# Performance work log

Measured on AMD Instinct MI355X. Metric: run time of the kernel, lower is better.

The kernel has to match this reference:

```python
import jax, jax.numpy as jnp
import numpy as np

T, N, E, H, G, P = 8, 512, 64, 128, 4, 128
NS = 2.0  # neighbourhood_size


def _init(k, shape):
    fan_in = shape[-1]
    return jax.random.normal(k, shape, jnp.float32) / jnp.sqrt(jnp.float32(fan_in))


def setup_inputs() -> dict:
    key = jax.random.key(0)
    ks = jax.random.split(key, 12)
    return {
        "observed": jax.random.normal(ks[0], (T, N, 2), jnp.float32),
        "W_pos": _init(ks[1], (E, 2)), "b_pos": jnp.zeros((E,), jnp.float32),
        "W_pool": _init(ks[2], (P, G * G * H)), "b_pool": jnp.zeros((P,), jnp.float32),
        "W_ih_enc": _init(ks[3], (4 * H, E + P)), "b_ih_enc": jnp.zeros((4 * H,), jnp.float32),
        "W_hh_enc": _init(ks[4], (4 * H, H)), "b_hh_enc": jnp.zeros((4 * H,), jnp.float32),
        "W_ih_dec": _init(ks[5], (4 * H, E + P)), "b_ih_dec": jnp.zeros((4 * H,), jnp.float32),
        "W_hh_dec": _init(ks[6], (4 * H, H)), "b_hh_dec": jnp.zeros((4 * H,), jnp.float32),
        "W_out": _init(ks[7], (2, H)), "b_out": jnp.zeros((2,), jnp.float32),
        "n_predict": 12,
    }


def _impute(observed):
    # backfill leading gaps, forward-fill later gaps, zeros if never valid
    Tn, n, _ = observed.shape
    finite = jnp.isfinite(observed).all(-1)                       # [T,N]
    idx = jnp.where(finite, jnp.arange(Tn)[:, None], -1)
    last = jax.lax.associative_scan(jnp.maximum, idx, axis=0)     # last valid t' <= t
    first = jnp.argmax(finite, axis=0)                            # first valid t
    take = jnp.where(last >= 0, last, first[None, :])             # [T,N]
    obs = jnp.take_along_axis(observed, jnp.broadcast_to(take[:, :, None], (Tn, n, 2)), axis=0)
    return jnp.where(finite.any(0)[None, :, None], obs, 0.0)


def _social_pool(pos, hidden, W_pool, b_pool):
    # grid-cell binning + per-cell max pooling of neighbour hidden states
    n, h = hidden.shape
    half, cell = NS / 2.0, NS / G
    rel = pos[None, :, :] - pos[:, None, :]                       # [N,N,2] pos[j]-pos[i]
    fin_pos = jnp.isfinite(pos).all(-1)
    fin_hid = jnp.isfinite(hidden).all(-1)
    inr = (jnp.abs(rel) <= half).all(-1)
    eye = jnp.eye(n, dtype=bool)
    mask = inr & fin_pos[:, None] & fin_pos[None, :] & fin_hid[None, :] & (~eye)
    g = jnp.clip(jnp.floor((rel + half) / cell).astype(jnp.int32), 0, G - 1)  # [N,N,2]
    cid = g[..., 0] * G + g[..., 1]                               # gx*G+gy layout
    seg = jnp.where(mask, jnp.arange(n, dtype=jnp.int32)[:, None] * (G * G) + cid, n * G * G)
    seg = seg.reshape(-1)                                         # [N*N]
    data = jnp.broadcast_to(hidden[None], (n, n, h)).reshape(n * n, h)
    pooled = jax.ops.segment_max(data, seg, num_segments=n * G * G + 1)[: n * G * G]
    counts = jax.ops.segment_sum(jnp.ones((n * n,), jnp.float32), seg, num_segments=n * G * G + 1)[: n * G * G]
    pooled = jnp.where(counts[:, None] > 0, pooled, 0.0)          # empty cells -> zero_hidden
    grid = pooled.reshape(n, G * G * h)
    return jax.nn.relu(grid @ W_pool.T + b_pool)


def reference(observed, W_pos, b_pos, W_pool, b_pool,
              W_ih_enc, b_ih_enc, W_hh_enc, b_hh_enc,
              W_ih_dec, b_ih_dec, W_hh_dec, b_hh_dec,
              W_out, b_out, n_predict):
    obs = _impute(observed)
    n = obs.shape[1]

    def step(W_ih, b_ih, W_hh, b_hh, hs, cs, pos, prev):
        vel = pos - prev
        emb = jax.nn.relu(vel @ W_pos.T + b_pos)
        soc = _social_pool(pos, hs, W_pool, b_pool)
        x = jnp.concatenate([emb, soc], axis=1)
        gates = x @ W_ih.T + b_ih + hs @ W_hh.T + b_hh
        i, f, gg, o = jnp.split(gates, 4, axis=1)
        cs2 = jax.nn.sigmoid(f) * cs + jax.nn.sigmoid(i) * jnp.tanh(gg)
        hs2 = jax.nn.sigmoid(o) * jnp.tanh(cs2)
        nxt = pos + hs2 @ W_out.T + b_out
        return hs2, cs2, nxt

    def enc_step(carry, inp):
        hs, cs = carry
        pos, prev = inp
        hs, cs, _ = step(W_ih_enc, b_ih_enc, W_hh_enc, b_hh_enc, hs, cs, pos, prev)
        return (hs, cs), None

    hs = jnp.zeros((n, H), jnp.float32)
    cs = jnp.zeros((n, H), jnp.float32)
    (hs, cs), _ = jax.lax.scan(enc_step, (hs, cs), (obs[1:], obs[:-1]))

    def dec_step(carry, _):
        hs, cs, prev, curr = carry
        hs, cs, nxt = step(W_ih_dec, b_ih_dec, W_hh_dec, b_hh_dec, hs, cs, curr, prev)
        return (hs, cs, jax.lax.stop_gradient(curr), jax.lax.stop_gradient(nxt)), nxt

    _, preds = jax.lax.scan(dec_step, (hs, cs, obs[-1], obs[-1]), None, length=int(n_predict))
    return preds  # [n_predict, N, 2]
```

## Files before the change

kernel.cpp:

```cpp
#include <hip/hip_runtime.h>
#include <math.h>

#define NBLK 256
#define NTHR 512

#define OFF_OBS     8256
#define OFF_HS      16448
#define OFF_PART    81984
#define OFF_WTPOOL  606272
#define OFF_WTG_E   868416
#define OFF_WTG_D   1032256

#define LDS_BYTES 31232

typedef float vf4 __attribute__((ext_vector_type(4)));
typedef float vf2 __attribute__((ext_vector_type(2)));

__device__ __forceinline__ int asr20(int row) { return row * 20 + ((row >> 5) << 2); }

__device__ __forceinline__ void st_bypass_f4(float* p, vf4 v) {
    asm volatile("global_store_dwordx4 %0, %1, off sc0 sc1" :: "v"(p), "v"(v) : "memory");
}
__device__ __forceinline__ void st_bypass_f2(float* p, vf2 v) {
    asm volatile("global_store_dwordx2 %0, %1, off sc0 sc1" :: "v"(p), "v"(v) : "memory");
}
__device__ __forceinline__ vf4 ld_bypass_f4(const float* p) {
    vf4 v;
    asm volatile("global_load_dwordx4 %0, %1, off sc0 sc1\n\ts_waitcnt vmcnt(0)"
                 : "=&v"(v) : "v"(p) : "memory");
    return v;
}
__device__ __forceinline__ void ld_bypass_f4x8(const float* b, int stride, vf4* v) {
    asm volatile(
        "global_load_dwordx4 %0, %8, off sc0 sc1\n\t"
        "global_load_dwordx4 %1, %9, off sc0 sc1\n\t"
        "global_load_dwordx4 %2, %10, off sc0 sc1\n\t"
        "global_load_dwordx4 %3, %11, off sc0 sc1\n\t"
        "global_load_dwordx4 %4, %12, off sc0 sc1\n\t"
        "global_load_dwordx4 %5, %13, off sc0 sc1\n\t"
        "global_load_dwordx4 %6, %14, off sc0 sc1\n\t"
        "global_load_dwordx4 %7, %15, off sc0 sc1\n\t"
        "s_waitcnt vmcnt(0)"
        : "=&v"(v[0]), "=&v"(v[1]), "=&v"(v[2]), "=&v"(v[3]),
          "=&v"(v[4]), "=&v"(v[5]), "=&v"(v[6]), "=&v"(v[7])
        : "v"(b), "v"(b + stride), "v"(b + 2 * stride), "v"(b + 3 * stride),
          "v"(b + 4 * stride), "v"(b + 5 * stride), "v"(b + 6 * stride), "v"(b + 7 * stride)
        : "memory");
}
__device__ __forceinline__ void ld_gather8(
    const float* a0, const float* a1, const float* a2, const float* a3,
    const float* a4, const float* a5, const float* a6, const float* a7, vf4* v) {
    asm volatile(
        "global_load_dwordx4 %0, %16, off sc0 sc1\n\t"
        "global_load_dwordx4 %1, %16, off offset:16 sc0 sc1\n\t"
        "global_load_dwordx4 %2, %17, off sc0 sc1\n\t"
        "global_load_dwordx4 %3, %17, off offset:16 sc0 sc1\n\t"
        "global_load_dwordx4 %4, %18, off sc0 sc1\n\t"
        "global_load_dwordx4 %5, %18, off offset:16 sc0 sc1\n\t"
        "global_load_dwordx4 %6, %19, off sc0 sc1\n\t"
        "global_load_dwordx4 %7, %19, off offset:16 sc0 sc1\n\t"
        "global_load_dwordx4 %8, %20, off sc0 sc1\n\t"
        "global_load_dwordx4 %9, %20, off offset:16 sc0 sc1\n\t"
        "global_load_dwordx4 %10, %21, off sc0 sc1\n\t"
        "global_load_dwordx4 %11, %21, off offset:16 sc0 sc1\n\t"
        "global_load_dwordx4 %12, %22, off sc0 sc1\n\t"
        "global_load_dwordx4 %13, %22, off offset:16 sc0 sc1\n\t"
        "global_load_dwordx4 %14, %23, off sc0 sc1\n\t"
        "global_load_dwordx4 %15, %23, off offset:16 sc0 sc1\n\t"
        "s_waitcnt vmcnt(0)"
        : "=&v"(v[0]), "=&v"(v[1]), "=&v"(v[2]), "=&v"(v[3]),
          "=&v"(v[4]), "=&v"(v[5]), "=&v"(v[6]), "=&v"(v[7]),
          "=&v"(v[8]), "=&v"(v[9]), "=&v"(v[10]), "=&v"(v[11]),
          "=&v"(v[12]), "=&v"(v[13]), "=&v"(v[14]), "=&v"(v[15])
        : "v"(a0), "v"(a1), "v"(a2), "v"(a3), "v"(a4), "v"(a5), "v"(a6), "v"(a7)
        : "memory");
}
__device__ __forceinline__ float ld_cohere(const float* p) {
    return __hip_atomic_load(p, __ATOMIC_RELAXED, __HIP_MEMORY_SCOPE_AGENT);
}

__device__ __forceinline__ void grid_barrier_fenced(unsigned* flags, unsigned* gen, unsigned seq) {
    __syncthreads();
    if (threadIdx.x == 0)
        __builtin_amdgcn_fence(__ATOMIC_RELEASE, "agent");
    if (blockIdx.x == 0) {
        if (threadIdx.x < 64) {
            #pragma unroll
            for (int q = 0; q < 4; q++) {
                int bb = threadIdx.x * 4 + q;
                if (bb != 0) {
                    while (__hip_atomic_load(&flags[bb * 16], __ATOMIC_RELAXED,
                                             __HIP_MEMORY_SCOPE_AGENT) != seq)
                        __builtin_amdgcn_s_sleep(1);
                }
            }
        }
        __syncthreads();
        if (threadIdx.x == 0) {
            __hip_atomic_store(gen, seq, __ATOMIC_RELAXED, __HIP_MEMORY_SCOPE_AGENT);
            __builtin_amdgcn_fence(__ATOMIC_ACQUIRE, "agent");
        }
    } else {
        if (threadIdx.x == 0) {
            __hip_atomic_store(&flags[blockIdx.x * 16], seq, __ATOMIC_RELAXED,
                               __HIP_MEMORY_SCOPE_AGENT);
            while (__hip_atomic_load(gen, __ATOMIC_RELAXED,
                                     __HIP_MEMORY_SCOPE_AGENT) != seq)
                __builtin_amdgcn_s_sleep(2);
            __builtin_amdgcn_fence(__ATOMIC_ACQUIRE, "agent");
        }
    }
    __syncthreads();
}

__device__ __forceinline__ void grid_barrier_nf(unsigned* flags, unsigned* gen, unsigned seq) {
    __syncthreads();
    if (blockIdx.x == 0) {
        if (threadIdx.x < 64) {
            #pragma unroll
            for (int q = 0; q < 4; q++) {
                int bb = threadIdx.x * 4 + q;
                if (bb != 0) {
                    while (__hip_atomic_load(&flags[bb * 16], __ATOMIC_RELAXED,
                                             __HIP_MEMORY_SCOPE_AGENT) != seq)
                        __builtin_amdgcn_s_sleep(1);
                }
            }
        }
        __syncthreads();
        if (threadIdx.x == 0)
            __hip_atomic_store(gen, seq, __ATOMIC_RELAXED, __HIP_MEMORY_SCOPE_AGENT);
    } else {
        if (threadIdx.x == 0) {
            __hip_atomic_store(&flags[blockIdx.x * 16], seq, __ATOMIC_RELAXED,
                               __HIP_MEMORY_SCOPE_AGENT);
            while (__hip_atomic_load(gen, __ATOMIC_RELAXED,
                                     __HIP_MEMORY_SCOPE_AGENT) != seq)
                __builtin_amdgcn_s_sleep(2);
        }
    }
    __syncthreads();
}

__device__ __forceinline__ float sigm(float x) { return 1.f / (1.f + expf(-x)); }

__global__ void __launch_bounds__(NTHR, 1) social_lstm(
    const float* __restrict__ observed,
    const float* __restrict__ W_pos, const float* __restrict__ b_pos,
    const float* __restrict__ W_pool, const float* __restrict__ b_pool,
    const float* __restrict__ Wih_e, const float* __restrict__ bih_e,
    const float* __restrict__ Whh_e, const float* __restrict__ bhh_e,
    const float* __restrict__ Wih_d, const float* __restrict__ bih_d,
    const float* __restrict__ Whh_d, const float* __restrict__ bhh_d,
    const float* __restrict__ W_out, const float* __restrict__ b_out,
    float* __restrict__ out, float* __restrict__ ws, int npred)
{
    extern __shared__ char smem_raw[];
    const int t = threadIdx.x, b = blockIdx.x;
    const int gid = b * NTHR + t;

    unsigned* flags  = (unsigned*)ws;
    unsigned* gen    = flags + 4096;
    unsigned* rtf    = flags + 4112;
    float* obs     = ws + OFF_OBS;
    float* hs      = ws + OFF_HS;
    float* part    = ws + OFF_PART;
    float* Wt_pool = ws + OFF_WTPOOL;
    float* Wt_ge   = ws + OFF_WTG_E;
    float* Wt_gd   = ws + OFF_WTG_D;
    unsigned seq = 1;

    if (gid < 65536) hs[gid] = 0.f;
    if (gid < 512) {
        float vx[8], vy[8];
        int fin = 0;
        for (int tt = 0; tt < 8; tt++) {
            float x = observed[tt * 1024 + gid * 2];
            float y = observed[tt * 1024 + gid * 2 + 1];
            vx[tt] = x; vy[tt] = y;
            if (isfinite(x) && isfinite(y)) fin |= (1 << tt);
        }
        int firstv = -1;
        for (int tt = 7; tt >= 0; tt--) if (fin & (1 << tt)) firstv = tt;
        int last = -1;
        for (int tt = 0; tt < 8; tt++) {
            if (fin & (1 << tt)) last = tt;
            int take = (last >= 0) ? last : firstv;
            float ox = 0.f, oy = 0.f;
            if (take >= 0) { ox = vx[take]; oy = vy[take]; }
            obs[tt * 1024 + gid * 2]     = ox;
            obs[tt * 1024 + gid * 2 + 1] = oy;
        }
    }
    if (gid < 65536) {
        int p = gid >> 9, k4 = gid & 511;
        float4 v = *(const float4*)(W_pool + p * 2048 + k4 * 4);
        float* dst = Wt_pool + (k4 * 4) * 128 + p;
        dst[0] = v.x; dst[128] = v.y; dst[256] = v.z; dst[384] = v.w;
    }
    for (int idx = gid; idx < 163840; idx += NBLK * NTHR) {
        int k = idx >> 9, o = idx & 511;
        float ve, vd;
        if (k < 192) { ve = Wih_e[o * 192 + k];       vd = Wih_d[o * 192 + k]; }
        else         { ve = Whh_e[o * 128 + k - 192]; vd = Whh_d[o * 128 + k - 192]; }
        Wt_ge[idx] = ve; Wt_gd[idx] = vd;
    }
    grid_barrier_fenced(flags, gen, seq++);

    const int rt = b >> 3, kc = b & 7, hc = kc;
    const int R0 = rt * 16;
    float cs_reg = 0.f;
    const int nstep = 7 + npred;

    for (int s = 0; s < nstep; s++) {
        const float* posp  = (s < 7) ? (obs + (s + 1) * 1024)
                                     : ((s == 7) ? (obs + 7 * 1024) : (out + (s - 8) * 1024));
        const float* prevp = (s < 7) ? (obs + s * 1024)
                                     : ((s <= 8) ? (obs + 7 * 1024) : (out + (s - 9) * 1024));
        const float* Wt_g = (s < 7) ? Wt_ge : Wt_gd;
        const float* bihp = (s < 7) ? bih_e : bih_d;
        const float* bhhp = (s < 7) ? bhh_e : bhh_d;

        {
            float* pos2 = (float*)smem_raw;
            int* cnt    = (int*)(smem_raw + 4096);
            unsigned short* lst = (unsigned short*)(smem_raw + 4224);
            float* AsT  = (float*)(smem_raw + 10368);

            if (t < 256) {
                if (s < 8) ((float4*)pos2)[t] = ((const float4*)posp)[t];
                else       ((vf4*)pos2)[t] = ld_bypass_f4(posp + t * 4);
            }
            if (t < 32) cnt[t] = 0;
            __syncthreads();

            if (kc == 1 && s >= 7 && t < 16) {
                int i = R0 + t;
                vf2 v;
                v.x = pos2[2 * i] + b_out[0];
                v.y = pos2[2 * i + 1] + b_out[1];
                st_bypass_f2(out + (s - 7) * 1024 + 2 * i, v);
            }
            {
                int a = t >> 5, i = R0 + a;
                float pix = pos2[2 * i], piy = pos2[2 * i + 1];
                int c0 = kc * 2;
                for (int jj = 0; jj < 16; jj++) {
                    int j = (t & 31) + jj * 32;
                    float dx = pos2[2 * j]     - pix;
                    float dy = pos2[2 * j + 1] - piy;
                    if (j != i && fabsf(dx) <= 1.0f && fabsf(dy) <= 1.0f) {
                        int gx = (int)floorf((dx + 1.0f) * 2.0f); gx = gx < 0 ? 0 : (gx > 3 ? 3 : gx);
                        int gy = (int)floorf((dy + 1.0f) * 2.0f); gy = gy < 0 ? 0 : (gy > 3 ? 3 : gy);
                        int cc = gx * 4 + gy - c0;
                        if (cc == 0 || cc == 1) {
                            int slot = atomicAdd(&cnt[a * 2 + cc], 1);
                            if (slot < 96) lst[(a * 2 + cc) * 96 + slot] = (unsigned short)j;
                        }
                    }
                }
            }
            __syncthreads();
            {
                int a = t >> 5, cc = (t >> 4) & 1, hq = t & 15;
                int len = cnt[a * 2 + cc]; if (len > 96) len = 96;
                float m[8];
                #pragma unroll
                for (int u = 0; u < 8; u++) m[u] = -3.0e38f;
                const unsigned short* ll = lst + (a * 2 + cc) * 96;
                for (int e = 0; e < len; e += 8) {
                    const float* ap[8];
                    #pragma unroll
                    for (int k2 = 0; k2 < 8; k2++) {
                        int ee = e + k2; if (ee >= len) ee = len - 1;
                        ap[k2] = hs + (int)ll[ee] * 128 + hq * 8;
                    }
                    vf4 v[16];
                    ld_gather8(ap[0], ap[1], ap[2], ap[3], ap[4], ap[5], ap[6], ap[7], v);
                    #pragma unroll
                    for (int k2 = 0; k2 < 8; k2++) {
                        vf4 lo = v[2 * k2], hi = v[2 * k2 + 1];
                        m[0] = fmaxf(m[0], lo.x); m[1] = fmaxf(m[1], lo.y);
                        m[2] = fmaxf(m[2], lo.z); m[3] = fmaxf(m[3], lo.w);
                        m[4] = fmaxf(m[4], hi.x); m[5] = fmaxf(m[5], hi.y);
                        m[6] = fmaxf(m[6], hi.z); m[7] = fmaxf(m[7], hi.w);
                    }
                }
                #pragma unroll
                for (int u = 0; u < 8; u++)
                    AsT[asr20(cc * 128 + hq * 8 + u) + a] = (len > 0) ? m[u] : 0.f;
            }
            __syncthreads();
            {
                int og = (t & 7) | (((t >> 6) & 1) << 3);
                int ks = (t >> 3) & 7;
                int rowg = t >> 7;
                float acc[4][8];
                #pragma unroll
                for (int r = 0; r < 4; r++)
                    #pragma unroll
                    for (int o = 0; o < 8; o++) acc[r][o] = 0.f;
                const float4* W4 = (const float4*)Wt_pool;
                int kb = kc * 256 + ks * 32;
                #pragma unroll 4
                for (int kk = 0; kk < 32; kk++) {
                    int kl = ks * 32 + kk;
                    float4 a4 = *(const float4*)&AsT[asr20(kl) + rowg * 4];
                    float4 w0 = W4[(kb + kk) * 32 + og * 2];
                    float4 w1 = W4[(kb + kk) * 32 + og * 2 + 1];
                    float ar[4] = {a4.x, a4.y, a4.z, a4.w};
                    float wo[8] = {w0.x, w0.y, w0.z, w0.w, w1.x, w1.y, w1.z, w1.w};
                    #pragma unroll
                    for (int r = 0; r < 4; r++)
                        #pragma unroll
                        for (int o = 0; o < 8; o++)
                            acc[r][o] = fmaf(ar[r], wo[o], acc[r][o]);
                }
                #pragma unroll
                for (int r = 0; r < 4; r++)
                    #pragma unroll
                    for (int o = 0; o < 8; o++) {
                        acc[r][o] += __shfl_xor(acc[r][o], 8);
                        acc[r][o] += __shfl_xor(acc[r][o], 16);
                        acc[r][o] += __shfl_xor(acc[r][o], 32);
                    }
                if ((t & 56) == 0) {
                    #pragma unroll
                    for (int r = 0; r < 4; r++) {
                        int row = R0 + rowg * 4 + r;
                        float* pp = part + kc * 65536 + row * 128 + og * 8;
                        vf4 lo, hi;
                        lo.x = acc[r][0]; lo.y = acc[r][1]; lo.z = acc[r][2]; lo.w = acc[r][3];
                        hi.x = acc[r][4]; hi.y = acc[r][5]; hi.z = acc[r][6]; hi.w = acc[r][7];
                        st_bypass_f4(pp,     lo);
                        st_bypass_f4(pp + 4, hi);
                    }
                }
            }
        }

        __syncthreads();
        if (t == 0)
            __hip_atomic_store(&rtf[(rt * 8 + kc) * 16], (unsigned)(s + 1),
                               __ATOMIC_RELAXED, __HIP_MEMORY_SCOPE_AGENT);
        {
            float* AsT  = (float*)smem_raw;
            {
                int r = t >> 5, e2 = (t & 31) * 2;
                int i2 = 2 * (R0 + r);
                float vx = ld_cohere(posp + i2)     - ld_cohere(prevp + i2);
                float vy = ld_cohere(posp + i2 + 1) - ld_cohere(prevp + i2 + 1);
                float e0 = fmaxf(W_pos[e2 * 2]     * vx + W_pos[e2 * 2 + 1] * vy + b_pos[e2],     0.f);
                float e1 = fmaxf(W_pos[e2 * 2 + 2] * vx + W_pos[e2 * 2 + 3] * vy + b_pos[e2 + 1], 0.f);
                AsT[asr20(e2 + 0) + r] = e0;
                AsT[asr20(e2 + 1) + r] = e1;
            }
            {
                int r = t >> 5, h4 = (t & 31) * 4;
                vf4 v = ld_bypass_f4(hs + (R0 + r) * 128 + h4);
                AsT[asr20(192 + h4 + 0) + r] = v.x;
                AsT[asr20(192 + h4 + 1) + r] = v.y;
                AsT[asr20(192 + h4 + 2) + r] = v.z;
                AsT[asr20(192 + h4 + 3) + r] = v.w;
            }
            if (t < 8) {
                while (__hip_atomic_load(&rtf[(rt * 8 + t) * 16], __ATOMIC_RELAXED,
                                         __HIP_MEMORY_SCOPE_AGENT) != (unsigned)(s + 1))
                    __builtin_amdgcn_s_sleep(1);
            }
            __syncthreads();
            {
                int r = t >> 5, p4 = (t & 31) * 4;
                vf4 pv[8];
                ld_bypass_f4x8(part + (R0 + r) * 128 + p4, 65536, pv);
                float sv[4] = {0.f, 0.f, 0.f, 0.f};
                #pragma unroll
                for (int kc2 = 0; kc2 < 8; kc2++) {
                    sv[0] += pv[kc2].x; sv[1] += pv[kc2].y;
                    sv[2] += pv[kc2].z; sv[3] += pv[kc2].w;
                }
                #pragma unroll
                for (int u = 0; u < 4; u++)
                    AsT[asr20(64 + p4 + u) + r] = fmaxf(sv[u] + b_pool[p4 + u], 0.f);
            }
            __syncthreads();
            float* red  = (float*)(smem_raw + 25792);
            float* hrow = (float*)(smem_raw + 29888);
            {
                int og = (t & 7) | (((t >> 6) & 1) << 3);
                int ks = (t >> 3) & 7;
                int rowg = t >> 7;
                int col4 = (og >> 2) * 32 + hc * 4 + (og & 3);
                float acc[4][4];
                #pragma unroll
                for (int r = 0; r < 4; r++)
                    #pragma unroll
                    for (int o = 0; o < 4; o++) acc[r][o] = 0.f;
                const float4* Wg4 = (const float4*)Wt_g;
                #pragma unroll 4
                for (int kk = 0; kk < 40; kk++) {
                    int k = ks * 40 + kk;
                    float4 a4 = *(const float4*)&AsT[asr20(k) + rowg * 4];
                    float4 w  = Wg4[k * 128 + col4];
                    float ar[4] = {a4.x, a4.y, a4.z, a4.w};
                    float wo[4] = {w.x, w.y, w.z, w.w};
                    #pragma unroll
                    for (int r = 0; r < 4; r++)
                        #pragma unroll
                        for (int o = 0; o < 4; o++)
                            acc[r][o] = fmaf(ar[r], wo[o], acc[r][o]);
                }
                #pragma unroll
                for (int r = 0; r < 4; r++)
                    #pragma unroll
                    for (int o = 0; o < 4; o++) {
                        acc[r][o] += __shfl_xor(acc[r][o], 8);
                        acc[r][o] += __shfl_xor(acc[r][o], 16);
                        acc[r][o] += __shfl_xor(acc[r][o], 32);
                    }
                if ((t & 56) == 0) {
                    #pragma unroll
                    for (int r = 0; r < 4; r++)
                        *(float4*)&red[(rowg * 4 + r) * 64 + og * 4] =
                            make_float4(acc[r][0], acc[r][1], acc[r][2], acc[r][3]);
                }
            }
            __syncthreads();
            if (t < 256) {
                int rl = t >> 4, hh = t & 15;
                float g4[4];
                #pragma unroll
                for (int q = 0; q < 4; q++) {
                    int colq = q * 128 + hc * 16 + hh;
                    g4[q] = red[rl * 64 + q * 16 + hh] + bihp[colq] + bhhp[colq];
                }
                float si = sigm(g4[0]);
                float sf = sigm(g4[1]);
                float so = sigm(g4[3]);
                float c2 = sf * cs_reg + si * tanhf(g4[2]);
                float h2 = so * tanhf(c2);
                cs_reg = c2;
                hrow[rl * 16 + hh] = h2;
                if (s >= 7) {
                    int i = R0 + rl, h = hc * 16 + hh;
                    float v0 = W_out[h] * h2;
                    float v1 = W_out[128 + h] * h2;
                    v0 += __shfl_down(v0, 8); v0 += __shfl_down(v0, 4);
                    v0 += __shfl_down(v0, 2); v0 += __shfl_down(v0, 1);
                    v1 += __shfl_down(v1, 8); v1 += __shfl_down(v1, 4);
                    v1 += __shfl_down(v1, 2); v1 += __shfl_down(v1, 1);
                    if (hh == 0) {
                        atomicAdd(&out[(s - 7) * 1024 + 2 * i],     v0);
                        atomicAdd(&out[(s - 7) * 1024 + 2 * i + 1], v1);
                    }
                }
            }
            __syncthreads();
            if (t < 64) {
                int rl = t >> 2, q = t & 3;
                vf4 v;
                v.x = hrow[rl * 16 + q * 4 + 0];
                v.y = hrow[rl * 16 + q * 4 + 1];
                v.z = hrow[rl * 16 + q * 4 + 2];
                v.w = hrow[rl * 16 + q * 4 + 3];
                st_bypass_f4(hs + (R0 + rl) * 128 + hc * 16 + q * 4, v);
            }
        }
        grid_barrier_nf(flags, gen, seq++);
    }
}

extern "C" void kernel_launch(void* const* d_in, const int* in_sizes, int n_in,
                              void* d_out, int out_size, void* d_ws, size_t ws_size,
                              hipStream_t stream) {
    const float* observed = (const float*)d_in[0];
    const float* W_pos    = (const float*)d_in[1];
    const float* b_pos    = (const float*)d_in[2];
    const float* W_pool   = (const float*)d_in[3];
    const float* b_pool   = (const float*)d_in[4];
    const float* Wih_e    = (const float*)d_in[5];
    const float* bih_e    = (const float*)d_in[6];
    const float* Whh_e    = (const float*)d_in[7];
    const float* bhh_e    = (const float*)d_in[8];
    const float* Wih_d    = (const float*)d_in[9];
    const float* bih_d    = (const float*)d_in[10];
    const float* Whh_d    = (const float*)d_in[11];
    const float* bhh_d    = (const float*)d_in[12];
    const float* W_out    = (const float*)d_in[13];
    const float* b_out    = (const float*)d_in[14];
    float* outp = (float*)d_out;
    float* wsp  = (float*)d_ws;
    int npred = out_size / 1024;

    hipMemsetAsync(d_ws, 0, 33024, stream);

    social_lstm<<<NBLK, NTHR, LDS_BYTES, stream>>>(
        observed, W_pos, b_pos, W_pool, b_pool,
        Wih_e, bih_e, Whh_e, bhh_e,
        Wih_d, bih_d, Whh_d, bhh_d,
        W_out, b_out, outp, wsp, npred);
}
```

Before: 640.6 us.

## Use per-step hidden-state buffers so reads can use cached loads

Replaces the single in-place hidden-state buffer with one separate buffer per time step. Each step reads the previous step's buffer and writes a fresh one. Because no address is ever rewritten, the gather, hidden-state and position loads drop their cache-bypassing asm and coherent atomic loads and become ordinary cached loads. The cost is more workspace, and correctness now depends on stale cache lines never aliasing a reused address, which could break if the workspace is reused across calls without invalidation.

```diff
diff --git a/kernel.cpp b/kernel.cpp
--- a/kernel.cpp
+++ b/kernel.cpp
@@ -5,11 +5,11 @@
 #define NTHR 512
 
 #define OFF_OBS     8256
-#define OFF_HS      16448
-#define OFF_PART    81984
-#define OFF_WTPOOL  606272
-#define OFF_WTG_E   868416
-#define OFF_WTG_D   1032256
+#define OFF_PART    16448
+#define OFF_WTPOOL  540736
+#define OFF_WTG_E   802880
+#define OFF_WTG_D   966720
+#define OFF_HSBUF   1130560
 
 #define LDS_BYTES 31232
 
@@ -23,12 +23,6 @@
 }
 __device__ __forceinline__ void st_bypass_f2(float* p, vf2 v) {
     asm volatile("global_store_dwordx2 %0, %1, off sc0 sc1" :: "v"(p), "v"(v) : "memory");
-}
-__device__ __forceinline__ vf4 ld_bypass_f4(const float* p) {
-    vf4 v;
-    asm volatile("global_load_dwordx4 %0, %1, off sc0 sc1\n\ts_waitcnt vmcnt(0)"
-                 : "=&v"(v) : "v"(p) : "memory");
-    return v;
 }
 __device__ __forceinline__ void ld_bypass_f4x8(const float* b, int stride, vf4* v) {
     asm volatile(
@@ -47,37 +41,6 @@
           "v"(b + 4 * stride), "v"(b + 5 * stride), "v"(b + 6 * stride), "v"(b + 7 * stride)
         : "memory");
 }
-__device__ __forceinline__ void ld_gather8(
-    const float* a0, const float* a1, const float* a2, const float* a3,
-    const float* a4, const float* a5, const float* a6, const float* a7, vf4* v) {
-    asm volatile(
-        "global_load_dwordx4 %0, %16, off sc0 sc1\n\t"
-        "global_load_dwordx4 %1, %16, off offset:16 sc0 sc1\n\t"
-        "global_load_dwordx4 %2, %17, off sc0 sc1\n\t"
-        "global_load_dwordx4 %3, %17, off offset:16 sc0 sc1\n\t"
-        "global_load_dwordx4 %4, %18, off sc0 sc1\n\t"
-        "global_load_dwordx4 %5, %18, off offset:16 sc0 sc1\n\t"
-        "global_load_dwordx4 %6, %19, off sc0 sc1\n\t"
-        "global_load_dwordx4 %7, %19, off offset:16 sc0 sc1\n\t"
-        "global_load_dwordx4 %8, %20, off sc0 sc1\n\t"
-        "global_load_dwordx4 %9, %20, off offset:16 sc0 sc1\n\t"
-        "global_load_dwordx4 %10, %21, off sc0 sc1\n\t"
-        "global_load_dwordx4 %11, %21, off offset:16 sc0 sc1\n\t"
-        "global_load_dwordx4 %12, %22, off sc0 sc1\n\t"
-        "global_load_dwordx4 %13, %22, off offset:16 sc0 sc1\n\t"
-        "global_load_dwordx4 %14, %23, off sc0 sc1\n\t"
-        "global_load_dwordx4 %15, %23, off offset:16 sc0 sc1\n\t"
-        "s_waitcnt vmcnt(0)"
-        : "=&v"(v[0]), "=&v"(v[1]), "=&v"(v[2]), "=&v"(v[3]),
-          "=&v"(v[4]), "=&v"(v[5]), "=&v"(v[6]), "=&v"(v[7]),
-          "=&v"(v[8]), "=&v"(v[9]), "=&v"(v[10]), "=&v"(v[11]),
-          "=&v"(v[12]), "=&v"(v[13]), "=&v"(v[14]), "=&v"(v[15])
-        : "v"(a0), "v"(a1), "v"(a2), "v"(a3), "v"(a4), "v"(a5), "v"(a6), "v"(a7)
-        : "memory");
-}
-__device__ __forceinline__ float ld_cohere(const float* p) {
-    return __hip_atomic_load(p, __ATOMIC_RELAXED, __HIP_MEMORY_SCOPE_AGENT);
-}
 
 __device__ __forceinline__ void grid_barrier_fenced(unsigned* flags, unsigned* gen, unsigned seq) {
     __syncthreads();
@@ -163,14 +126,14 @@
     unsigned* gen    = flags + 4096;
     unsigned* rtf    = flags + 4112;
     float* obs     = ws + OFF_OBS;
-    float* hs      = ws + OFF_HS;
     float* part    = ws + OFF_PART;
     float* Wt_pool = ws + OFF_WTPOOL;
     float* Wt_ge   = ws + OFF_WTG_E;
     float* Wt_gd   = ws + OFF_WTG_D;
+    float* hsbuf   = ws + OFF_HSBUF;
     unsigned seq = 1;
 
-    if (gid < 65536) hs[gid] = 0.f;
+    if (gid < 65536) hsbuf[gid] = 0.f;
     if (gid < 512) {
         float vx[8], vy[8];
         int fin = 0;
@@ -220,6 +183,8 @@
         const float* Wt_g = (s < 7) ? Wt_ge : Wt_gd;
         const float* bihp = (s < 7) ? bih_e : bih_d;
         const float* bhhp = (s < 7) ? bhh_e : bhh_d;
+        const float* hs_r = hsbuf + s * 65536;
+        float*       hs_w = hsbuf + (s + 1) * 65536;
 
         {
             float* pos2 = (float*)smem_raw;
@@ -227,10 +192,7 @@
             unsigned short* lst = (unsigned short*)(smem_raw + 4224);
             float* AsT  = (float*)(smem_raw + 10368);
 
-            if (t < 256) {
-                if (s < 8) ((float4*)pos2)[t] = ((const float4*)posp)[t];
-                else       ((vf4*)pos2)[t] = ld_bypass_f4(posp + t * 4);
-            }
+            if (t < 256) ((float4*)pos2)[t] = ((const float4*)posp)[t];
             if (t < 32) cnt[t] = 0;
             __syncthreads();
 
@@ -269,21 +231,19 @@
                 for (int u = 0; u < 8; u++) m[u] = -3.0e38f;
                 const unsigned short* ll = lst + (a * 2 + cc) * 96;
                 for (int e = 0; e < len; e += 8) {
-                    const float* ap[8];
+                    float4 va[8], vb[8];
                     #pragma unroll
                     for (int k2 = 0; k2 < 8; k2++) {
                         int ee = e + k2; if (ee >= len) ee = len - 1;
-                        ap[k2] = hs + (int)ll[ee] * 128 + hq * 8;
-                    }
-                    vf4 v[16];
-                    ld_gather8(ap[0], ap[1], ap[2], ap[3], ap[4], ap[5], ap[6], ap[7], v);
+                        const float4* hp = (const float4*)(hs_r + (int)ll[ee] * 128 + hq * 8);
+                        va[k2] = hp[0]; vb[k2] = hp[1];
+                    }
                     #pragma unroll
                     for (int k2 = 0; k2 < 8; k2++) {
-                        vf4 lo = v[2 * k2], hi = v[2 * k2 + 1];
-                        m[0] = fmaxf(m[0], lo.x); m[1] = fmaxf(m[1], lo.y);
-                        m[2] = fmaxf(m[2], lo.z); m[3] = fmaxf(m[3], lo.w);
-                        m[4] = fmaxf(m[4], hi.x); m[5] = fmaxf(m[5], hi.y);
-                        m[6] = fmaxf(m[6], hi.z); m[7] = fmaxf(m[7], hi.w);
+                        m[0] = fmaxf(m[0], va[k2].x); m[1] = fmaxf(m[1], va[k2].y);
+                        m[2] = fmaxf(m[2], va[k2].z); m[3] = fmaxf(m[3], va[k2].w);
+                        m[4] = fmaxf(m[4], vb[k2].x); m[5] = fmaxf(m[5], vb[k2].y);
+                        m[6] = fmaxf(m[6], vb[k2].z); m[7] = fmaxf(m[7], vb[k2].w);
                     }
                 }
                 #pragma unroll
@@ -348,8 +308,8 @@
             {
                 int r = t >> 5, e2 = (t & 31) * 2;
                 int i2 = 2 * (R0 + r);
-                float vx = ld_cohere(posp + i2)     - ld_cohere(prevp + i2);
-                float vy = ld_cohere(posp + i2 + 1) - ld_cohere(prevp + i2 + 1);
+                float vx = posp[i2]     - prevp[i2];
+                float vy = posp[i2 + 1] - prevp[i2 + 1];
                 float e0 = fmaxf(W_pos[e2 * 2]     * vx + W_pos[e2 * 2 + 1] * vy + b_pos[e2],     0.f);
                 float e1 = fmaxf(W_pos[e2 * 2 + 2] * vx + W_pos[e2 * 2 + 3] * vy + b_pos[e2 + 1], 0.f);
                 AsT[asr20(e2 + 0) + r] = e0;
@@ -357,7 +317,7 @@
             }
             {
                 int r = t >> 5, h4 = (t & 31) * 4;
-                vf4 v = ld_bypass_f4(hs + (R0 + r) * 128 + h4);
+                float4 v = *(const float4*)(hs_r + (R0 + r) * 128 + h4);
                 AsT[asr20(192 + h4 + 0) + r] = v.x;
                 AsT[asr20(192 + h4 + 1) + r] = v.y;
                 AsT[asr20(192 + h4 + 2) + r] = v.z;
@@ -463,7 +423,7 @@
                 v.y = hrow[rl * 16 + q * 4 + 1];
                 v.z = hrow[rl * 16 + q * 4 + 2];
                 v.w = hrow[rl * 16 + q * 4 + 3];
-                st_bypass_f4(hs + (R0 + rl) * 128 + hc * 16 + q * 4, v);
+                st_bypass_f4(hs_w + (R0 + rl) * 128 + hc * 16 + q * 4, v);
             }
         }
         grid_barrier_nf(flags, gen, seq++);
```

After: 606.5 us. 5.3% less time.
